# Kernel optimization log

Hardware: AMD Instinct MI355X
Metric: run time of the kernel (lower is better)

## Reference

```python
import jax, jax.numpy as jnp
import numpy as np

UNITS = 128
HEADS = 8
D_IN = 1024
BATCH = 4
SEQ = 2048


def setup_inputs() -> dict:
    key = jax.random.key(0)
    ks = jax.random.split(key, 9)
    s = 1.0 / np.sqrt(D_IN)
    return {
        "x": jax.random.normal(ks[0], (BATCH, SEQ, D_IN), dtype=jnp.float32),
        "query_kernel": jax.random.normal(ks[1], (HEADS, D_IN, UNITS), dtype=jnp.float32) * s,
        "key_kernel": jax.random.normal(ks[2], (HEADS, D_IN, UNITS), dtype=jnp.float32) * s,
        "value_kernel": jax.random.normal(ks[3], (HEADS, D_IN, UNITS), dtype=jnp.float32) * s,
        "query_bias": jnp.zeros((HEADS, UNITS), dtype=jnp.float32),
        "key_bias": jnp.zeros((HEADS, UNITS), dtype=jnp.float32),
        "value_bias": jnp.zeros((HEADS, UNITS), dtype=jnp.float32),
        "head_kernel": jax.random.normal(ks[7], (HEADS * UNITS, UNITS), dtype=jnp.float32) * (1.0 / np.sqrt(HEADS * UNITS)),
        "head_bias": jnp.zeros((UNITS,), dtype=jnp.float32),
    }


def reference(x, query_kernel, key_kernel, value_kernel, query_bias, key_bias, value_bias, head_kernel, head_bias):
    # x: [B, S, D]; per-head projections -> [B, H, S, U]
    q = jnp.einsum("bsd,hdu->bhsu", x, query_kernel) + query_bias[None, :, None, :]
    k = jnp.einsum("bsd,hdu->bhsu", x, key_kernel) + key_bias[None, :, None, :]
    v = jnp.einsum("bsd,hdu->bhsu", x, value_kernel) + value_bias[None, :, None, :]
    scale = 1.0 / np.sqrt(UNITS).astype(np.float32)
    sims = jnp.einsum("bhsu,bhtu->bhst", q, k) * scale  # [B, H, S, S]
    attn = jax.nn.softmax(sims, axis=-1)
    weighted = jnp.einsum("bhst,bhtu->bhsu", attn, v)  # [B, H, S, U]
    b, h, s, u = weighted.shape
    flat = jnp.transpose(weighted, (0, 2, 1, 3)).reshape(b, s, h * u)  # [B, S, H*U]
    out = flat @ head_kernel + head_bias  # [B, S, U]
    return out  # activation is linear (None)
```

## Files before the change

### kernel.cpp

```cpp
#include <hip/hip_runtime.h>
#include <math.h>

#define BB 4
#define SS 2048
#define DD 1024
#define HH 8
#define UU 128
#define NTOK (BB*SS)
#define SCALE_LOG2E 0.12751779f

typedef __attribute__((ext_vector_type(4))) float f32x4;
typedef __attribute__((ext_vector_type(8))) short s16x8;

__device__ __forceinline__ unsigned short bf16_rn(float f) {
    unsigned u = __float_as_uint(f);
    u += 0x7FFFu + ((u >> 16) & 1u);
    return (unsigned short)(u >> 16);
}
__device__ __forceinline__ float bf16_f32(unsigned short h) {
    return __uint_as_float(((unsigned)h) << 16);
}

#define MFMA16(a,b,c) __builtin_amdgcn_mfma_f32_16x16x32_bf16((a),(b),(c),0,0,0)

__device__ __forceinline__ void gll16(const unsigned short* g, unsigned short* l) {
    __builtin_amdgcn_global_load_lds(
        (const __attribute__((address_space(1))) unsigned int*)g,
        (__attribute__((address_space(3))) unsigned int*)l,
        16, 0, 0);
}

__global__ __launch_bounds__(256) void convert_x(
    const float* __restrict__ x, unsigned short* __restrict__ xs)
{
    const int NCH = NTOK*DD/4;
    for (int idx = blockIdx.x*256 + threadIdx.x; idx < NCH; idx += 2048*256) {
        int r  = idx >> 8;
        int c4 = (idx & 255) * 4;
        float4 v = *(const float4*)(x + (size_t)r*DD + c4);
        short4 H;
        H.x = (short)bf16_rn(v.x);
        H.y = (short)bf16_rn(v.y);
        H.z = (short)bf16_rn(v.z);
        H.w = (short)bf16_rn(v.w);
        *(short4*)(xs + (size_t)r*DD + c4) = H;
    }
}

__global__ __launch_bounds__(256) void convert_w(
    const float* __restrict__ wq, const float* __restrict__ wk, const float* __restrict__ wv,
    const float* __restrict__ wh,
    unsigned short* __restrict__ ws, unsigned short* __restrict__ whd)
{
    const int dt = blockIdx.x;
    const int z  = blockIdx.y;
    const float* src;
    if (z < 8)       { src = wq + (size_t)z*DD*UU; }
    else if (z < 16) { src = wk + (size_t)(z-8)*DD*UU; }
    else if (z < 24) { src = wv + (size_t)(z-16)*DD*UU; }
    else             { src = wh; }

    __shared__ float T[64][132];
    const int t = threadIdx.x;
    const int d0 = dt*64;
    #pragma unroll
    for (int i = 0; i < 8; ++i) {
        int ch = i*256 + t;
        int r  = ch >> 5;
        int c4 = (ch & 31) * 4;
        float4 v = *(const float4*)(src + (size_t)(d0 + r)*UU + c4);
        T[r][c4+0]=v.x; T[r][c4+1]=v.y; T[r][c4+2]=v.z; T[r][c4+3]=v.w;
    }
    __syncthreads();
    #pragma unroll
    for (int i = 0; i < 4; ++i) {
        int ch = i*256 + t;
        int u  = ch >> 3;
        int d8 = (ch & 7) * 8;
        s16x8 H, L;
        #pragma unroll
        for (int j = 0; j < 8; ++j) {
            float f = T[d8+j][u];
            unsigned short hh = bf16_rn(f);
            H[j] = (short)hh;
            L[j] = (short)bf16_rn(f - bf16_f32(hh));
        }
        if (z < 24) {
            *(s16x8*)(ws + (size_t)(z*128 + u)*1024 + d0 + d8) = H;
        } else {
            size_t off = (size_t)u*3072 + d0 + d8;
            *(s16x8*)(whd + off)        = H;
            *(s16x8*)(whd + off + 1024) = L;
            *(s16x8*)(whd + off + 2048) = H;
        }
    }
}

__global__ __launch_bounds__(256) void qkv_gemm(
    const unsigned short* __restrict__ xs, const unsigned short* __restrict__ ws,
    const float* __restrict__ bq, const float* __restrict__ bk, const float* __restrict__ bv,
    unsigned short* __restrict__ q_hi,
    unsigned short* __restrict__ k_hi,
    unsigned short* __restrict__ vt_hi)
{
    const int wg  = blockIdx.x;
    const int sw  = (wg & 7)*192 + (wg >> 3);
    const int xcd = sw / 192;
    const int idx = sw - xcd*192;
    const int nt  = xcd*3 + (idx % 3);
    const int mt  = idx / 3;
    const int which = nt >> 3;
    const int h  = nt & 7;

    __shared__ __align__(16) short As[128*64], Bs[128*64];

    const int t    = threadIdx.x;
    const int wid  = t >> 6;
    const int lane = t & 63;
    const int wm = wid >> 1, wn = wid & 1;
    const int l15 = lane & 15, lg = lane >> 4;

    f32x4 acc[4][4];
    const f32x4 fz = {0.f,0.f,0.f,0.f};
    #pragma unroll
    for (int i = 0; i < 4; ++i)
        #pragma unroll
        for (int j = 0; j < 4; ++j) acc[i][j] = fz;

    const unsigned short* abase = xs + (size_t)mt*128*1024;
    const unsigned short* bbase = ws + (size_t)nt*128*1024;

    for (int k0 = 0; k0 < 1024; k0 += 64) {
        __syncthreads();
        #pragma unroll
        for (int i = 0; i < 4; ++i) {
            int slot = wid*256 + i*64 + lane;
            int r = slot >> 3, c = slot & 7;
            gll16(abase + (size_t)r*1024 + k0 + ((c ^ (r & 7))*8),
                  (unsigned short*)&As[(wid*256 + i*64)*8]);
        }
        #pragma unroll
        for (int i = 0; i < 4; ++i) {
            int slot = wid*256 + i*64 + lane;
            int r = slot >> 3, c = slot & 7;
            gll16(bbase + (size_t)r*1024 + k0 + ((c ^ (r & 7))*8),
                  (unsigned short*)&Bs[(wid*256 + i*64)*8]);
        }
        __syncthreads();

        #pragma unroll
        for (int ks = 0; ks < 2; ++ks) {
            const int kb = ks*32 + lg*8;
            s16x8 av[4], bv2[4];
            #pragma unroll
            for (int mf = 0; mf < 4; ++mf) {
                int r = wm*64 + mf*16 + l15;
                av[mf] = *(const s16x8*)(&As[r*64 + (kb ^ ((r & 7) << 3))]);
            }
            #pragma unroll
            for (int nf = 0; nf < 4; ++nf) {
                int r = wn*64 + nf*16 + l15;
                bv2[nf] = *(const s16x8*)(&Bs[r*64 + (kb ^ ((r & 7) << 3))]);
            }
            #pragma unroll
            for (int mf = 0; mf < 4; ++mf)
                #pragma unroll
                for (int nf = 0; nf < 4; ++nf)
                    acc[mf][nf] = MFMA16(av[mf], bv2[nf], acc[mf][nf]);
        }
    }

    const float* bias = (which==0) ? bq : (which==1) ? bk : bv;
    #pragma unroll
    for (int nf = 0; nf < 4; ++nf) {
        int u = wn*64 + nf*16 + l15;
        float bb = bias[h*UU + u];
        #pragma unroll
        for (int mf = 0; mf < 4; ++mf) {
            int m0 = mt*128 + wm*64 + mf*16 + lg*4;
            int b  = m0 >> 11;
            int s  = m0 & (SS-1);
            size_t bhb = (size_t)(b*HH + h);
            if (which == 0) {
                #pragma unroll
                for (int rg = 0; rg < 4; ++rg)
                    q_hi[(bhb*SS + (s + rg))*UU + u] = bf16_rn(acc[mf][nf][rg] + bb);
            } else if (which == 1) {
                #pragma unroll
                for (int rg = 0; rg < 4; ++rg)
                    k_hi[(bhb*SS + (s + rg))*UU + u] = bf16_rn(acc[mf][nf][rg] + bb);
            } else {
                short4 pk;
                pk.x = (short)bf16_rn(acc[mf][nf][0] + bb);
                pk.y = (short)bf16_rn(acc[mf][nf][1] + bb);
                pk.z = (short)bf16_rn(acc[mf][nf][2] + bb);
                pk.w = (short)bf16_rn(acc[mf][nf][3] + bb);
                *(short4*)(vt_hi + (bhb*UU + u)*SS + s) = pk;
            }
        }
    }
}

__global__ __launch_bounds__(512, 2) void attn(
    const unsigned short* __restrict__ q_hi,
    const unsigned short* __restrict__ k_hi,
    const unsigned short* __restrict__ vt_hi,
    unsigned short* __restrict__ flat_hi, unsigned short* __restrict__ flat_lo)
{
    const int wg = blockIdx.x;
    const int sw = (wg & 7)*32 + (wg >> 3);
    const int b  = sw >> 6;
    const int h  = (sw >> 3) & 7;
    const int qt = sw & 7;
    const size_t bh = (size_t)(b*HH + h);

    __shared__ __align__(16) short KH[2][64*128];
    __shared__ __align__(16) short VT[2][128*64];
    __shared__ __align__(16) short PL[8][32*72];

    const int t    = threadIdx.x;
    const int wid  = t >> 6;
    const int lane = t & 63;
    const int l15 = lane & 15, lg = lane >> 4;

    const unsigned short* kbase = k_hi  + bh*SS*UU;
    const unsigned short* vbase = vt_hi + bh*UU*SS;

    s16x8 qh[2][4];
    #pragma unroll
    for (int mf = 0; mf < 2; ++mf) {
        int r = qt*256 + wid*32 + mf*16 + l15;
        const unsigned short* qrh = q_hi + (bh*SS + r)*UU + lg*8;
        #pragma unroll
        for (int ks = 0; ks < 4; ++ks)
            qh[mf][ks] = *(const s16x8*)(qrh + ks*32);
    }

    f32x4 accO[2][8];
    const f32x4 fz = {0.f,0.f,0.f,0.f};
    float m_run[2], l_run[2];
    #pragma unroll
    for (int mf = 0; mf < 2; ++mf) {
        #pragma unroll
        for (int nf = 0; nf < 8; ++nf) accO[mf][nf] = fz;
        m_run[mf] = -INFINITY; l_run[mf] = 0.f;
    }

    {
        const int base_ = wid*128;
        #pragma unroll
        for (int i_ = 0; i_ < 2; ++i_) {
            int slot = base_ + i_*64 + lane;
            int r_ = slot >> 4, c_ = slot & 15;
            gll16(kbase + ((size_t)r_)*UU + ((c_ ^ (r_ & 7))*8),
                  (unsigned short*)&KH[0][(base_ + i_*64)*8]);
        }
        #pragma unroll
        for (int i_ = 0; i_ < 2; ++i_) {
            int slot = base_ + i_*64 + lane;
            int u_ = slot >> 3, c_ = slot & 7;
            gll16(vbase + ((size_t)u_)*SS + ((c_ ^ (u_ & 7))*8),
                  (unsigned short*)&VT[0][(base_ + i_*64)*8]);
        }
    }
    __syncthreads();

    short* P = PL[wid];

    for (int kt = 0; kt < SS/64; ++kt) {
        const int cur = kt & 1;
        if (kt + 1 < SS/64) {
            const int nxt = cur ^ 1;
            const int base_ = wid*128;
            #pragma unroll
            for (int i_ = 0; i_ < 2; ++i_) {
                int slot = base_ + i_*64 + lane;
                int r_ = slot >> 4, c_ = slot & 15;
                gll16(kbase + ((size_t)((kt+1)*64 + r_))*UU + ((c_ ^ (r_ & 7))*8),
                      (unsigned short*)&KH[nxt][(base_ + i_*64)*8]);
            }
            #pragma unroll
            for (int i_ = 0; i_ < 2; ++i_) {
                int slot = base_ + i_*64 + lane;
                int u_ = slot >> 3, c_ = slot & 7;
                gll16(vbase + ((size_t)u_)*SS + (kt+1)*64 + ((c_ ^ (u_ & 7))*8),
                      (unsigned short*)&VT[nxt][(base_ + i_*64)*8]);
            }
        }

        f32x4 sacc[4][2];
        #pragma unroll
        for (int kf = 0; kf < 4; ++kf)
            #pragma unroll
            for (int qf = 0; qf < 2; ++qf) sacc[kf][qf] = fz;
        __builtin_amdgcn_s_setprio(1);
        #pragma unroll
        for (int ks = 0; ks < 4; ++ks) {
            const int kb = ks*32 + lg*8;
            s16x8 kh_[4];
            #pragma unroll
            for (int kf = 0; kf < 4; ++kf) {
                int r = kf*16 + l15;
                kh_[kf] = *(const s16x8*)(&KH[cur][r*128 + (kb ^ ((r & 7) << 3))]);
            }
            #pragma unroll
            for (int kf = 0; kf < 4; ++kf)
                #pragma unroll
                for (int qf = 0; qf < 2; ++qf)
                    sacc[kf][qf] = MFMA16(kh_[kf], qh[qf][ks], sacc[kf][qf]);
        }
        __builtin_amdgcn_s_setprio(0);

        float mx[2];
        #pragma unroll
        for (int qf = 0; qf < 2; ++qf) {
            f32x4 m4 = sacc[0][qf];
            #pragma unroll
            for (int kf = 1; kf < 4; ++kf) {
                m4[0] = fmaxf(m4[0], sacc[kf][qf][0]);
                m4[1] = fmaxf(m4[1], sacc[kf][qf][1]);
                m4[2] = fmaxf(m4[2], sacc[kf][qf][2]);
                m4[3] = fmaxf(m4[3], sacc[kf][qf][3]);
            }
            float mq = fmaxf(fmaxf(m4[0], m4[1]), fmaxf(m4[2], m4[3])) * SCALE_LOG2E;
            mq = fmaxf(mq, __shfl_xor(mq, 16, 64));
            mq = fmaxf(mq, __shfl_xor(mq, 32, 64));
            mx[qf] = mq;
        }
        float need = fmaxf(mx[0] - m_run[0], mx[1] - m_run[1]);
        if (__any(need > 8.0f)) {
            float fq[2];
            #pragma unroll
            for (int qf = 0; qf < 2; ++qf) {
                float mn = fmaxf(m_run[qf], mx[qf]);
                fq[qf] = exp2f(m_run[qf] - mn);
                m_run[qf] = mn;
                l_run[qf] *= fq[qf];
            }
            #pragma unroll
            for (int mf = 0; mf < 2; ++mf)
                #pragma unroll
                for (int rg = 0; rg < 4; ++rg) {
                    float fa = __shfl(fq[mf], (lg*4 + rg) | (lane & 48), 64);
                    #pragma unroll
                    for (int nf = 0; nf < 8; ++nf) accO[mf][nf][rg] *= fa;
                }
        }
        #pragma unroll
        for (int qf = 0; qf < 2; ++qf) {
            float sum = 0.f;
            #pragma unroll
            for (int kf = 0; kf < 4; ++kf)
                #pragma unroll
                for (int rg = 0; rg < 4; ++rg) {
                    float p = exp2f(sacc[kf][qf][rg]*SCALE_LOG2E - m_run[qf]);
                    sacc[kf][qf][rg] = p;
                    sum += p;
                }
            sum += __shfl_xor(sum, 16, 64);
            sum += __shfl_xor(sum, 32, 64);
            l_run[qf] += sum;
        }

        #pragma unroll
        for (int qf = 0; qf < 2; ++qf)
            #pragma unroll
            for (int kf = 0; kf < 4; ++kf) {
                short4 pk;
                pk.x = (short)bf16_rn(sacc[kf][qf][0]);
                pk.y = (short)bf16_rn(sacc[kf][qf][1]);
                pk.z = (short)bf16_rn(sacc[kf][qf][2]);
                pk.w = (short)bf16_rn(sacc[kf][qf][3]);
                *(short4*)&P[(qf*16 + l15)*72 + kf*16 + lg*4] = pk;
            }

        __builtin_amdgcn_s_setprio(1);
        #pragma unroll
        for (int ks = 0; ks < 2; ++ks) {
            const int kb = ks*32 + lg*8;
            s16x8 pa[2], vb[8];
            #pragma unroll
            for (int mf = 0; mf < 2; ++mf)
                pa[mf] = *(const s16x8*)(P + (mf*16 + l15)*72 + kb);
            #pragma unroll
            for (int nf = 0; nf < 8; ++nf) {
                int u = nf*16 + l15;
                vb[nf] = *(const s16x8*)(&VT[cur][u*64 + (kb ^ ((u & 7) << 3))]);
            }
            #pragma unroll
            for (int mf = 0; mf < 2; ++mf)
                #pragma unroll
                for (int nf = 0; nf < 8; ++nf)
                    accO[mf][nf] = MFMA16(pa[mf], vb[nf], accO[mf][nf]);
        }
        __builtin_amdgcn_s_setprio(0);

        __syncthreads();
    }

    #pragma unroll
    for (int mf = 0; mf < 2; ++mf) {
        float invq = 1.0f / l_run[mf];
        #pragma unroll
        for (int rg = 0; rg < 4; ++rg) {
            float inv = __shfl(invq, (lg*4 + rg) | (lane & 48), 64);
            int srow = qt*256 + wid*32 + mf*16 + lg*4 + rg;
            size_t nrow = (size_t)b*SS + srow;
            #pragma unroll
            for (int nf = 0; nf < 8; ++nf) {
                float ov = accO[mf][nf][rg] * inv;
                unsigned short hh = bf16_rn(ov);
                size_t o = nrow*(size_t)(HH*UU) + h*UU + nf*16 + l15;
                flat_hi[o] = hh;
                flat_lo[o] = bf16_rn(ov - bf16_f32(hh));
            }
        }
    }
}

__global__ __launch_bounds__(256) void final_gemm(
    const unsigned short* __restrict__ fh, const unsigned short* __restrict__ fl,
    const unsigned short* __restrict__ whd,
    const float* __restrict__ bias, float* __restrict__ out)
{
    const int mt = blockIdx.x;

    __shared__ __align__(16) short As[2][32*64], Bs[2][128*64];

    const int t    = threadIdx.x;
    const int wid  = t >> 6;
    const int lane = t & 63;
    const int l15 = lane & 15, lg = lane >> 4;

    f32x4 acc[2][2];
    const f32x4 fz = {0.f,0.f,0.f,0.f};
    #pragma unroll
    for (int i = 0; i < 2; ++i)
        #pragma unroll
        for (int j = 0; j < 2; ++j) acc[i][j] = fz;

    #define FSTAGE(buf, k0_) do {                                                 \
        const unsigned short* src_; int kk_;                                      \
        if ((k0_) < 1024)      { src_ = fh; kk_ = (k0_); }                        \
        else if ((k0_) < 2048) { src_ = fh; kk_ = (k0_) - 1024; }                 \
        else                   { src_ = fl; kk_ = (k0_) - 2048; }                 \
        { int slot = wid*64 + lane; int r = slot >> 3, c = slot & 7;              \
          gll16(src_ + (size_t)(mt*32 + r)*DD + kk_ + ((c ^ (r & 7))*8),          \
                (unsigned short*)&As[buf][(wid*64)*8]); }                         \
        _Pragma("unroll")                                                         \
        for (int i_ = 0; i_ < 4; ++i_) {                                          \
          int slot = wid*256 + i_*64 + lane; int r = slot >> 3, c = slot & 7;     \
          gll16(whd + (size_t)r*3072 + (k0_) + ((c ^ (r & 7))*8),                 \
                (unsigned short*)&Bs[buf][(wid*256 + i_*64)*8]); }                \
    } while (0)

    FSTAGE(0, 0);
    __syncthreads();

    for (int step = 0; step < 48; ++step) {
        const int cur = step & 1;
        if (step + 1 < 48) FSTAGE(cur ^ 1, (step + 1)*64);

        #pragma unroll
        for (int ks = 0; ks < 2; ++ks) {
            const int kb = ks*32 + lg*8;
            s16x8 av[2], bv2[2];
            #pragma unroll
            for (int mf = 0; mf < 2; ++mf) {
                int r = mf*16 + l15;
                av[mf] = *(const s16x8*)(&As[cur][r*64 + (kb ^ ((r & 7) << 3))]);
            }
            #pragma unroll
            for (int nf = 0; nf < 2; ++nf) {
                int r = wid*32 + nf*16 + l15;
                bv2[nf] = *(const s16x8*)(&Bs[cur][r*64 + (kb ^ ((r & 7) << 3))]);
            }
            #pragma unroll
            for (int mf = 0; mf < 2; ++mf)
                #pragma unroll
                for (int nf = 0; nf < 2; ++nf)
                    acc[mf][nf] = MFMA16(av[mf], bv2[nf], acc[mf][nf]);
        }
        __syncthreads();
    }
    #undef FSTAGE

    #pragma unroll
    for (int nf = 0; nf < 2; ++nf) {
        int u = wid*32 + nf*16 + l15;
        float bb = bias[u];
        #pragma unroll
        for (int mf = 0; mf < 2; ++mf) {
            int m0 = mt*32 + mf*16 + lg*4;
            #pragma unroll
            for (int rg = 0; rg < 4; ++rg)
                out[(size_t)(m0 + rg)*UU + u] = acc[mf][nf][rg] + bb;
        }
    }
}

extern "C" void kernel_launch(void* const* d_in, const int* in_sizes, int n_in,
                              void* d_out, int out_size, void* d_ws, size_t ws_size,
                              hipStream_t stream) {
    const float* x     = (const float*)d_in[0];
    const float* wq    = (const float*)d_in[1];
    const float* wk    = (const float*)d_in[2];
    const float* wv    = (const float*)d_in[3];
    const float* bq    = (const float*)d_in[4];
    const float* bk    = (const float*)d_in[5];
    const float* bv    = (const float*)d_in[6];
    const float* whead = (const float*)d_in[7];
    const float* bhead = (const float*)d_in[8];

    unsigned short* p = (unsigned short*)d_ws;
    const size_t SEG = (size_t)BB*HH*SS*UU;
    unsigned short* xs   = p;  p += (size_t)NTOK*DD;
    unsigned short* ws_g = p;  p += (size_t)3072*1024;
    unsigned short* whd  = p;  p += (size_t)128*3072;
    unsigned short* q_hi = p;  p += SEG;
    unsigned short* k_hi = p;  p += SEG;
    unsigned short* vt_hi = p; p += SEG;
    unsigned short* flat_hi = p; p += SEG;
    unsigned short* flat_lo = p; p += SEG;

    convert_x<<<2048, 256, 0, stream>>>(x, xs);
    convert_w<<<dim3(16, 25), 256, 0, stream>>>(wq, wk, wv, whead, ws_g, whd);
    qkv_gemm<<<1536, 256, 0, stream>>>(xs, ws_g, bq, bk, bv,
                                       q_hi, k_hi, vt_hi);
    attn<<<256, 512, 0, stream>>>(q_hi, k_hi, vt_hi, flat_hi, flat_lo);
    final_gemm<<<256, 256, 0, stream>>>(flat_hi, flat_lo, whd, bhead,
                                        (float*)d_out);
}
```

Baseline: 307.8 us.

## Split attention into 512 smaller blocks with packed bf16 convert and swizzled P

The attention kernel now launches 512 workgroups of 256 threads (4 waves) covering 128 query rows each, instead of 256 workgroups of 8 waves covering 256 rows. Each wave loads twice as much of the K/V tile per step. The P staging buffer drops its padding and uses an XOR swizzle instead, and the bf16 packing of probabilities now uses the hardware v_cvt_pk_bf16_f32 instruction. The aim is better load balance across CUs and cheaper conversions, but each K/V tile is now reused by fewer query rows, so total K/V traffic into LDS doubles.

```diff
diff --git a/kernel.cpp b/kernel.cpp
--- a/kernel.cpp
+++ b/kernel.cpp
@@ -19,6 +19,11 @@
 }
 __device__ __forceinline__ float bf16_f32(unsigned short h) {
     return __uint_as_float(((unsigned)h) << 16);
+}
+__device__ __forceinline__ unsigned cvt_pk_bf16(float lo, float hi) {
+    unsigned r;
+    asm("v_cvt_pk_bf16_f32 %0, %1, %2" : "=v"(r) : "v"(lo), "v"(hi));
+    return r;
 }
 
 #define MFMA16(a,b,c) __builtin_amdgcn_mfma_f32_16x16x32_bf16((a),(b),(c),0,0,0)
@@ -201,22 +206,22 @@
     }
 }
 
-__global__ __launch_bounds__(512, 2) void attn(
+__global__ __launch_bounds__(256, 2) void attn(
     const unsigned short* __restrict__ q_hi,
     const unsigned short* __restrict__ k_hi,
     const unsigned short* __restrict__ vt_hi,
     unsigned short* __restrict__ flat_hi, unsigned short* __restrict__ flat_lo)
 {
     const int wg = blockIdx.x;
-    const int sw = (wg & 7)*32 + (wg >> 3);
-    const int b  = sw >> 6;
-    const int h  = (sw >> 3) & 7;
-    const int qt = sw & 7;
+    const int sw = (wg & 7)*64 + (wg >> 3);
+    const int b  = sw >> 7;
+    const int h  = (sw >> 4) & 7;
+    const int qt = sw & 15;
     const size_t bh = (size_t)(b*HH + h);
 
     __shared__ __align__(16) short KH[2][64*128];
     __shared__ __align__(16) short VT[2][128*64];
-    __shared__ __align__(16) short PL[8][32*72];
+    __shared__ __align__(16) short PL[4][32*64];
 
     const int t    = threadIdx.x;
     const int wid  = t >> 6;
@@ -229,7 +234,7 @@
     s16x8 qh[2][4];
     #pragma unroll
     for (int mf = 0; mf < 2; ++mf) {
-        int r = qt*256 + wid*32 + mf*16 + l15;
+        int r = qt*128 + wid*32 + mf*16 + l15;
         const unsigned short* qrh = q_hi + (bh*SS + r)*UU + lg*8;
         #pragma unroll
         for (int ks = 0; ks < 4; ++ks)
@@ -247,20 +252,19 @@
     }
 
     {
-        const int base_ = wid*128;
-        #pragma unroll
-        for (int i_ = 0; i_ < 2; ++i_) {
-            int slot = base_ + i_*64 + lane;
+        #pragma unroll
+        for (int i_ = 0; i_ < 4; ++i_) {
+            int slot = wid*256 + i_*64 + lane;
             int r_ = slot >> 4, c_ = slot & 15;
             gll16(kbase + ((size_t)r_)*UU + ((c_ ^ (r_ & 7))*8),
-                  (unsigned short*)&KH[0][(base_ + i_*64)*8]);
-        }
-        #pragma unroll
-        for (int i_ = 0; i_ < 2; ++i_) {
-            int slot = base_ + i_*64 + lane;
+                  (unsigned short*)&KH[0][(wid*256 + i_*64)*8]);
+        }
+        #pragma unroll
+        for (int i_ = 0; i_ < 4; ++i_) {
+            int slot = wid*256 + i_*64 + lane;
             int u_ = slot >> 3, c_ = slot & 7;
             gll16(vbase + ((size_t)u_)*SS + ((c_ ^ (u_ & 7))*8),
-                  (unsigned short*)&VT[0][(base_ + i_*64)*8]);
+                  (unsigned short*)&VT[0][(wid*256 + i_*64)*8]);
         }
     }
     __syncthreads();
@@ -271,20 +275,19 @@
         const int cur = kt & 1;
         if (kt + 1 < SS/64) {
             const int nxt = cur ^ 1;
-            const int base_ = wid*128;
-            #pragma unroll
-            for (int i_ = 0; i_ < 2; ++i_) {
-                int slot = base_ + i_*64 + lane;
+            #pragma unroll
+            for (int i_ = 0; i_ < 4; ++i_) {
+                int slot = wid*256 + i_*64 + lane;
                 int r_ = slot >> 4, c_ = slot & 15;
                 gll16(kbase + ((size_t)((kt+1)*64 + r_))*UU + ((c_ ^ (r_ & 7))*8),
-                      (unsigned short*)&KH[nxt][(base_ + i_*64)*8]);
-            }
-            #pragma unroll
-            for (int i_ = 0; i_ < 2; ++i_) {
-                int slot = base_ + i_*64 + lane;
+                      (unsigned short*)&KH[nxt][(wid*256 + i_*64)*8]);
+            }
+            #pragma unroll
+            for (int i_ = 0; i_ < 4; ++i_) {
+                int slot = wid*256 + i_*64 + lane;
                 int u_ = slot >> 3, c_ = slot & 7;
                 gll16(vbase + ((size_t)u_)*SS + (kt+1)*64 + ((c_ ^ (u_ & 7))*8),
-                      (unsigned short*)&VT[nxt][(base_ + i_*64)*8]);
+                      (unsigned short*)&VT[nxt][(wid*256 + i_*64)*8]);
             }
         }
 
@@ -366,12 +369,11 @@
         for (int qf = 0; qf < 2; ++qf)
             #pragma unroll
             for (int kf = 0; kf < 4; ++kf) {
-                short4 pk;
-                pk.x = (short)bf16_rn(sacc[kf][qf][0]);
-                pk.y = (short)bf16_rn(sacc[kf][qf][1]);
-                pk.z = (short)bf16_rn(sacc[kf][qf][2]);
-                pk.w = (short)bf16_rn(sacc[kf][qf][3]);
-                *(short4*)&P[(qf*16 + l15)*72 + kf*16 + lg*4] = pk;
+                unsigned lo = cvt_pk_bf16(sacc[kf][qf][0], sacc[kf][qf][1]);
+                unsigned hi = cvt_pk_bf16(sacc[kf][qf][2], sacc[kf][qf][3]);
+                int row = qf*16 + l15;
+                int col = (kf*16 + lg*4) ^ ((l15 & 7) << 3);
+                *(uint2*)&P[row*64 + col] = make_uint2(lo, hi);
             }
 
         __builtin_amdgcn_s_setprio(1);
@@ -380,8 +382,10 @@
             const int kb = ks*32 + lg*8;
             s16x8 pa[2], vb[8];
             #pragma unroll
-            for (int mf = 0; mf < 2; ++mf)
-                pa[mf] = *(const s16x8*)(P + (mf*16 + l15)*72 + kb);
+            for (int mf = 0; mf < 2; ++mf) {
+                int r = mf*16 + l15;
+                pa[mf] = *(const s16x8*)(&P[r*64 + (kb ^ ((l15 & 7) << 3))]);
+            }
             #pragma unroll
             for (int nf = 0; nf < 8; ++nf) {
                 int u = nf*16 + l15;
@@ -404,7 +408,7 @@
         #pragma unroll
         for (int rg = 0; rg < 4; ++rg) {
             float inv = __shfl(invq, (lg*4 + rg) | (lane & 48), 64);
-            int srow = qt*256 + wid*32 + mf*16 + lg*4 + rg;
+            int srow = qt*128 + wid*32 + mf*16 + lg*4 + rg;
             size_t nrow = (size_t)b*SS + srow;
             #pragma unroll
             for (int nf = 0; nf < 8; ++nf) {
@@ -527,7 +531,7 @@
     convert_w<<<dim3(16, 25), 256, 0, stream>>>(wq, wk, wv, whead, ws_g, whd);
     qkv_gemm<<<1536, 256, 0, stream>>>(xs, ws_g, bq, bk, bv,
                                        q_hi, k_hi, vt_hi);
-    attn<<<256, 512, 0, stream>>>(q_hi, k_hi, vt_hi, flat_hi, flat_lo);
+    attn<<<512, 256, 0, stream>>>(q_hi, k_hi, vt_hi, flat_hi, flat_lo);
     final_gemm<<<256, 256, 0, stream>>>(flat_hi, flat_lo, whd, bhead,
                                         (float*)d_out);
 }
```

After: 305.2 us. About the same (-0.8%).
